# Kernel tuning notes

Hardware: AMD Instinct MI355X
Metric: run time of the kernel (lower is better)

## Reference

```python
import jax, jax.numpy as jnp
import numpy as np

NEG_SLOPE = 0.2
CONV3_NUM, CONV1_NUM, POLY_NUM = 3, 5, 4
FEAT_DIM = CONV3_NUM * 84 + CONV1_NUM * 12 + POLY_NUM * 12  # 360
DN = ('NCHW', 'OIHW', 'NCHW')


def leaky_relu(x):
    return jnp.where(x >= 0, x, NEG_SLOPE * x)


def conv3x3(x, feat):
    # per-sample dynamic 3x3 conv: feat[:, :81] -> kernel [3,3,3,3], feat[:, 81:84] -> bias
    B = x.shape[0]
    k = feat[:, :81].reshape(B, 3, 3, 3, 3)
    b = feat[:, 81:84]

    def one(xi, ki, bi):
        y = jax.lax.conv_general_dilated(xi[None], ki, (1, 1), 'SAME', dimension_numbers=DN)[0]
        return y + bi[:, None, None]

    return leaky_relu(jax.vmap(one)(x, k, b))


def conv1x1(x, feat):
    B = x.shape[0]
    k = feat[:, :9].reshape(B, 3, 3, 1, 1)
    b = feat[:, 9:12]

    def one(xi, ki, bi):
        y = jax.lax.conv_general_dilated(xi[None], ki, (1, 1), 'VALID', dimension_numbers=DN)[0]
        return y + bi[:, None, None]

    return leaky_relu(jax.vmap(one)(x, k, b))


def conv_stack(x, feature):
    residual = x
    for i in range(CONV3_NUM):
        x = conv3x3(x, feature[:, i * 84:(i + 1) * 84])
    off = CONV3_NUM * 84
    for i in range(CONV1_NUM):
        x = conv1x1(x, feature[:, off + i * 12:off + (i + 1) * 12])
    return residual + x


def att_map(feat, h_mat, w_mat, xc):
    # product over POLY_NUM of (a*h + b*w + c*x + d)
    att = jnp.ones_like(xc)
    for i in range(POLY_NUM):
        a = feat[:, i * 4 + 0].reshape(-1, 1, 1, 1)
        b = feat[:, i * 4 + 1].reshape(-1, 1, 1, 1)
        c = feat[:, i * 4 + 2].reshape(-1, 1, 1, 1)
        d = feat[:, i * 4 + 3].reshape(-1, 1, 1, 1)
        att = att * (a * h_mat + b * w_mat + c * xc + d)
    return att


def apply_attention(x, feature):
    H, W = x.shape[2], x.shape[3]
    h_mat = (jnp.arange(H, dtype=x.dtype) / H).reshape(1, 1, H, 1)
    w_mat = (jnp.arange(W, dtype=x.dtype) / W).reshape(1, 1, 1, W)
    off = CONV3_NUM * 84 + CONV1_NUM * 12
    atts = [att_map(feature[:, off + c * POLY_NUM * 4: off + (c + 1) * POLY_NUM * 4],
                    h_mat, w_mat, x[:, c:c + 1]) for c in range(3)]  # R, G, B
    att = jnp.concatenate(atts, axis=1)
    return x * (1 + att)


def setup_inputs() -> dict:
    key = jax.random.key(0)
    k1, k2, k3 = jax.random.split(key, 3)
    x = jax.random.uniform(k1, (8, 3, 512, 512), dtype=jnp.float32)
    thumb_x = jax.random.uniform(k2, (8, 3, 64, 64), dtype=jnp.float32)
    Wm = jax.random.normal(k3, (3, FEAT_DIM), dtype=jnp.float32) * 0.05
    bm = jnp.zeros((FEAT_DIM,), dtype=jnp.float32)
    return {"x": x, "thumb_x": thumb_x, "Wm": Wm, "bm": bm}


def reference(x, thumb_x, Wm, bm):
    # meta: GAP over thumbnail -> linear -> per-sample hypernetwork features [B, 360]
    feature = jnp.mean(thumb_x, axis=(2, 3)) @ Wm + bm
    x = conv_stack(x, feature)
    x = apply_attention(x, feature)
    thumb = conv_stack(thumb_x, feature)
    thumb = apply_attention(thumb, feature)
    return (x, thumb)
```

## Files before the change

kernel.cpp:

```cpp
#include <hip/hip_runtime.h>


typedef float v2f __attribute__((ext_vector_type(2)));
#define FMA2(a, b, c) __builtin_elementwise_fma((a), (b), (c))

__device__ __forceinline__ v2f leaky2(v2f v) {
    return __builtin_elementwise_max(v, v * 0.2f);
}

__device__ __forceinline__ v2f ldpair(const float* p) {
    v2f r; __builtin_memcpy(&r, p, 8); return r;
}
__device__ __forceinline__ void stpair(float* p, v2f v) {
    __builtin_memcpy(p, &v, 8);
}

constexpr int ROWS0 = 22;
constexpr int NCOLS = 73;
constexpr int CSTR  = 23;
constexpr int CHS   = NCOLS * CSTR;
constexpr int BUFSZ = 3 * CHS + 4;

__global__ __launch_bounds__(384) void prep_kernel(
    const float* __restrict__ thumb, const float* __restrict__ Wm,
    const float* __restrict__ bm, float* __restrict__ feat)
{
    const int b = blockIdx.x;
    const int t = threadIdx.x;
    const int ch = t >> 7;
    const int l  = t & 127;
    const float4* p = (const float4*)(thumb + (size_t)b * 3 * 4096);
    float s = 0.f;
#pragma unroll
    for (int k = 0; k < 8; ++k) {
        float4 v = p[ch * 1024 + l + k * 128];
        s += v.x + v.y + v.z + v.w;
    }
    __shared__ float red[384];
    red[t] = s;
    __syncthreads();
    for (int off = 64; off > 0; off >>= 1) {
        if (l < off) red[t] += red[t + off];
        __syncthreads();
    }
    if (t < 360) {
        const float sc = 1.f / 4096.f;
        const float m0 = red[0] * sc, m1 = red[128] * sc, m2 = red[256] * sc;
        feat[b * 360 + t] =
            fmaf(m0, Wm[t], fmaf(m1, Wm[360 + t], fmaf(m2, Wm[720 + t], bm[t])));
    }
}

__device__ __forceinline__ void conv_rows_pk(
    const float* __restrict__ buf, const float* __restrict__ fw,
    int r0, int gx, v2f acc[3][4])
{
    const float b0 = fw[81], b1 = fw[82], b2 = fw[83];
#pragma unroll
    for (int c = 0; c < 4; ++c) {
        v2f i0 = {b0, b0}; v2f i1 = {b1, b1}; v2f i2 = {b2, b2};
        acc[0][c] = i0; acc[1][c] = i1; acc[2][c] = i2;
    }
    const int c0 = (gx < 0) ? 3 : gx + 3;
    const int rb = r0 + 2;
#pragma unroll
    for (int ich = 0; ich < 3; ++ich) {
        const int base = ich * CHS + rb;
#pragma unroll
        for (int dy = 0; dy < 3; ++dy) {
            v2f win[6];
            win[0] = ldpair(&buf[base + c0 * CSTR + dy]);
#pragma unroll
            for (int k = 1; k < 6; ++k)
                win[k] = ldpair(&buf[base + (gx + 3 + k) * CSTR + dy]);
#pragma unroll
            for (int oc = 0; oc < 3; ++oc) {
                const float w0 = fw[oc * 27 + ich * 9 + dy * 3 + 0];
                const float w1 = fw[oc * 27 + ich * 9 + dy * 3 + 1];
                const float w2 = fw[oc * 27 + ich * 9 + dy * 3 + 2];
                v2f W0 = {w0, w0}; v2f W1 = {w1, w1}; v2f W2 = {w2, w2};
#pragma unroll
                for (int c = 0; c < 4; ++c) {
                    acc[oc][c] = FMA2(win[c], W0,
                                 FMA2(win[c + 1], W1,
                                 FMA2(win[c + 2], W2, acc[oc][c])));
                }
            }
        }
    }
}

__device__ __forceinline__ void write_strip_pk(
    float* __restrict__ buf, int r0, int gx, v2f acc[3][4])
{
#pragma unroll
    for (int oc = 0; oc < 3; ++oc)
#pragma unroll
        for (int c = 0; c < 4; ++c)
            stpair(&buf[oc * CHS + (gx + 4 + c) * CSTR + (r0 + 3)],
                   leaky2(acc[oc][c]));
}

__global__ __launch_bounds__(256, 4) void conv_att_kernel(
    const float* __restrict__ x, const float* __restrict__ thumb,
    const float* __restrict__ feat, float* __restrict__ out)
{
    __shared__ float buf[BUFSZ];

    int id = blockIdx.x;
    const float* src; float* dst; int H, W, b, trow, tcol;
    if (id < 2048) {
        b = id >> 8; const int t = id & 255;
        H = 512; W = 512; trow = (t >> 3) * 16; tcol = (t & 7) * 64;
        src = x; dst = out;
    } else {
        const int i2 = id - 2048;
        b = i2 >> 2; trow = (i2 & 3) * 16; tcol = 0;
        H = 64; W = 64; src = thumb;
        dst = out + (size_t)8 * 3 * 512 * 512;
    }
    const float* fb = feat + b * 360;
    const int tid = threadIdx.x;

    const float* sbg = src + (size_t)b * 3 * H * W;
    for (int q = tid; q < 1056; q += 256) {
        const int c = q / 352;
        const int rem = q - c * 352;
        const int mr = rem >> 4;
        const int k  = rem & 15;
        const int gr = trow + mr - 3;
        const int gc0 = tcol + 4 * k;
        float4 v = make_float4(0.f, 0.f, 0.f, 0.f);
        if ((unsigned)gr < (unsigned)H)
            v = *(const float4*)&sbg[(size_t)c * H * W + (size_t)gr * W + gc0];
        float* bp = &buf[c * CHS + (4 * k + 4) * CSTR + mr];
        bp[0] = v.x; bp[CSTR] = v.y; bp[2 * CSTR] = v.z; bp[3 * CSTR] = v.w;
    }
    if (tid < 132) {
        const int c = tid / 44;
        const int rem = tid - c * 44;
        const int mr = rem >> 1;
        const int side = rem & 1;
        const int gr = trow + mr - 3;
        const int gc0 = tcol + (side ? 64 : -4);
        const bool rok = (unsigned)gr < (unsigned)H;
        const float* gp = sbg + (size_t)c * H * W + (size_t)(rok ? gr : 0) * W;
        float4 v;
        if (rok && (unsigned)gc0 <= (unsigned)(W - 4)) {
            v = *(const float4*)&gp[gc0];
        } else {
            v.x = (rok && (unsigned)(gc0 + 0) < (unsigned)W) ? gp[gc0 + 0] : 0.f;
            v.y = (rok && (unsigned)(gc0 + 1) < (unsigned)W) ? gp[gc0 + 1] : 0.f;
            v.z = (rok && (unsigned)(gc0 + 2) < (unsigned)W) ? gp[gc0 + 2] : 0.f;
            v.w = (rok && (unsigned)(gc0 + 3) < (unsigned)W) ? gp[gc0 + 3] : 0.f;
        }
        float* bp = &buf[c * CHS + (side ? 68 : 0) * CSTR + mr];
        bp[0] = v.x; bp[CSTR] = v.y; bp[2 * CSTR] = v.z; bp[3 * CSTR] = v.w;
    }
    if (tid < 66) {
        const int c = tid / 22, mr = tid - c * 22;
        buf[c * CHS + 72 * CSTR + mr] = 0.f;
    }
    __syncthreads();

    const bool act1 = tid < 180;
    int s1, gx1;
    if (tid < 160) { s1 = tid >> 4; gx1 = 4 * (tid & 15); }
    else { const int v = tid - 160; s1 = v >> 1; gx1 = (v & 1) ? 64 : -4; }
    v2f acc[3][4];
    if (act1) conv_rows_pk(buf, fb, 2 * s1 - 2, gx1, acc);

    const int s3 = tid >> 4;
    const int gx3 = 4 * (tid & 15);
    v2f res2[3][4];
    if (tid < 128) {
#pragma unroll
        for (int ch = 0; ch < 3; ++ch)
#pragma unroll
            for (int c = 0; c < 4; ++c)
                res2[ch][c] = ldpair(&buf[ch * CHS + (gx3 + 4 + c) * CSTR + (2 * s3 + 3)]);
    }
    __syncthreads();

    if (act1) write_strip_pk(buf, 2 * s1 - 2, gx1, acc);
    __syncthreads();

    const bool act2 = tid < 162;
    int s2, gx2;
    if (tid < 144) { s2 = tid >> 4; gx2 = 4 * (tid & 15); }
    else { const int v = tid - 144; s2 = v >> 1; gx2 = (v & 1) ? 64 : -4; }
    if (act2) conv_rows_pk(buf, fb + 84, 2 * s2 - 1, gx2, acc);
    __syncthreads();

    if (act2) write_strip_pk(buf, 2 * s2 - 1, gx2, acc);
    __syncthreads();

    if (tid < 128) {
        v2f y[3][4];
        {
            v2f acc3[3][4];
            conv_rows_pk(buf, fb + 168, 2 * s3, gx3, acc3);
#pragma unroll
            for (int oc = 0; oc < 3; ++oc)
#pragma unroll
                for (int c = 0; c < 4; ++c) y[oc][c] = leaky2(acc3[oc][c]);
        }

#pragma unroll
        for (int lay = 0; lay < 5; ++lay) {
            const float* fw = fb + 252 + lay * 12;
            v2f W0 = {fw[0], fw[0]}; v2f W1 = {fw[1], fw[1]}; v2f W2 = {fw[2], fw[2]};
            v2f W3 = {fw[3], fw[3]}; v2f W4 = {fw[4], fw[4]}; v2f W5 = {fw[5], fw[5]};
            v2f W6 = {fw[6], fw[6]}; v2f W7 = {fw[7], fw[7]}; v2f W8 = {fw[8], fw[8]};
            v2f C0 = {fw[9], fw[9]}; v2f C1 = {fw[10], fw[10]}; v2f C2 = {fw[11], fw[11]};
            v2f z0[4], z1[4], z2[4];
#pragma unroll
            for (int c = 0; c < 4; ++c) {
                z0[c] = FMA2(y[0][c], W0, FMA2(y[1][c], W1, FMA2(y[2][c], W2, C0)));
                z1[c] = FMA2(y[0][c], W3, FMA2(y[1][c], W4, FMA2(y[2][c], W5, C1)));
                z2[c] = FMA2(y[0][c], W6, FMA2(y[1][c], W7, FMA2(y[2][c], W8, C2)));
            }
#pragma unroll
            for (int c = 0; c < 4; ++c) {
                y[0][c] = leaky2(z0[c]);
                y[1][c] = leaky2(z1[c]);
                y[2][c] = leaky2(z2[c]);
            }
        }

        const float invH = 1.f / (float)H;
        const float invW = 1.f / (float)W;
        const int gr0 = trow + 2 * s3;
        v2f h2 = {(float)gr0 * invH, (float)(gr0 + 1) * invH};
        const float wb = (float)(tcol + gx3) * invW;
        const v2f one = {1.f, 1.f};
#pragma unroll
        for (int ch = 0; ch < 3; ++ch) {
            const float* fp = fb + 312 + ch * 16;
            v2f PA0 = {fp[0], fp[0]},  PB0 = {fp[1], fp[1]},  PC0 = {fp[2], fp[2]},  PD0 = {fp[3], fp[3]};
            v2f PA1 = {fp[4], fp[4]},  PB1 = {fp[5], fp[5]},  PC1 = {fp[6], fp[6]},  PD1 = {fp[7], fp[7]};
            v2f PA2 = {fp[8], fp[8]},  PB2 = {fp[9], fp[9]},  PC2 = {fp[10], fp[10]}, PD2 = {fp[11], fp[11]};
            v2f PA3 = {fp[12], fp[12]}, PB3 = {fp[13], fp[13]}, PC3 = {fp[14], fp[14]}, PD3 = {fp[15], fp[15]};
            v2f t0 = FMA2(PA0, h2, PD0);
            v2f t1 = FMA2(PA1, h2, PD1);
            v2f t2 = FMA2(PA2, h2, PD2);
            v2f t3 = FMA2(PA3, h2, PD3);
            v2f o[4];
#pragma unroll
            for (int c = 0; c < 4; ++c) {
                const float wcs = wb + (float)c * invW;
                v2f Wc = {wcs, wcs};
                v2f v = y[ch][c] + res2[ch][c];
                v2f a = FMA2(PB0, Wc, FMA2(PC0, v, t0));
                a = a * FMA2(PB1, Wc, FMA2(PC1, v, t1));
                a = a * FMA2(PB2, Wc, FMA2(PC2, v, t2));
                a = a * FMA2(PB3, Wc, FMA2(PC3, v, t3));
                o[c] = v * (one + a);
            }
            float4 ra = make_float4(o[0].x, o[1].x, o[2].x, o[3].x);
            float4 rb = make_float4(o[0].y, o[1].y, o[2].y, o[3].y);
            float* dp = &dst[((size_t)(b * 3 + ch) * H + gr0) * W + tcol + gx3];
            *(float4*)dp = ra;
            *(float4*)(dp + W) = rb;
        }
    }
}

extern "C" void kernel_launch(void* const* d_in, const int* in_sizes, int n_in,
                              void* d_out, int out_size, void* d_ws, size_t ws_size,
                              hipStream_t stream) {
    const float* x = (const float*)d_in[0];
    const float* thumb = (const float*)d_in[1];
    const float* Wm = (const float*)d_in[2];
    const float* bm = (const float*)d_in[3];
    float* out = (float*)d_out;
    float* feat = (float*)d_ws;

    prep_kernel<<<8, 384, 0, stream>>>(thumb, Wm, bm, feat);
    conv_att_kernel<<<2080, 256, 0, stream>>>(x, thumb, feat, out);
}
```

Measured before the change: 111.7 us.

## Ping-pong conv layers between two shared buffers and batch global loads

Replaces the single in-place shared buffer with two buffers (A and B), so each 3x3 conv layer reads one and writes the other. This removes the extra barrier that was needed between computing and writing back each layer. The tile loads are also restructured so that all global float4 loads are issued into registers before any LDS stores, which improves memory-level parallelism. The cost is more shared memory per block, which could lower occupancy, plus more live registers during the load phase.

```diff
diff --git a/kernel.cpp b/kernel.cpp
--- a/kernel.cpp
+++ b/kernel.cpp
@@ -15,11 +15,13 @@
     __builtin_memcpy(p, &v, 8);
 }
 
-constexpr int ROWS0 = 22;
 constexpr int NCOLS = 73;
-constexpr int CSTR  = 23;
-constexpr int CHS   = NCOLS * CSTR;
-constexpr int BUFSZ = 3 * CHS + 4;
+constexpr int CSTRA = 23;
+constexpr int CHSA  = NCOLS * CSTRA;
+constexpr int ASZ   = 3 * CHSA + 4;
+constexpr int CSTRB = 21;
+constexpr int CHSB  = NCOLS * CSTRB;
+constexpr int BSZ   = 3 * CHSB + 4;
 
 __global__ __launch_bounds__(384) void prep_kernel(
     const float* __restrict__ thumb, const float* __restrict__ Wm,
@@ -51,9 +53,10 @@
     }
 }
 
+template<int CHS_, int CSTR_>
 __device__ __forceinline__ void conv_rows_pk(
     const float* __restrict__ buf, const float* __restrict__ fw,
-    int r0, int gx, v2f acc[3][4])
+    int rb, int gx, v2f acc[3][4])
 {
     const float b0 = fw[81], b1 = fw[82], b2 = fw[83];
 #pragma unroll
@@ -62,17 +65,16 @@
         acc[0][c] = i0; acc[1][c] = i1; acc[2][c] = i2;
     }
     const int c0 = (gx < 0) ? 3 : gx + 3;
-    const int rb = r0 + 2;
 #pragma unroll
     for (int ich = 0; ich < 3; ++ich) {
-        const int base = ich * CHS + rb;
+        const int base = ich * CHS_ + rb;
 #pragma unroll
         for (int dy = 0; dy < 3; ++dy) {
             v2f win[6];
-            win[0] = ldpair(&buf[base + c0 * CSTR + dy]);
+            win[0] = ldpair(&buf[base + c0 * CSTR_ + dy]);
 #pragma unroll
             for (int k = 1; k < 6; ++k)
-                win[k] = ldpair(&buf[base + (gx + 3 + k) * CSTR + dy]);
+                win[k] = ldpair(&buf[base + (gx + 3 + k) * CSTR_ + dy]);
 #pragma unroll
             for (int oc = 0; oc < 3; ++oc) {
                 const float w0 = fw[oc * 27 + ich * 9 + dy * 3 + 0];
@@ -90,22 +92,12 @@
     }
 }
 
-__device__ __forceinline__ void write_strip_pk(
-    float* __restrict__ buf, int r0, int gx, v2f acc[3][4])
-{
-#pragma unroll
-    for (int oc = 0; oc < 3; ++oc)
-#pragma unroll
-        for (int c = 0; c < 4; ++c)
-            stpair(&buf[oc * CHS + (gx + 4 + c) * CSTR + (r0 + 3)],
-                   leaky2(acc[oc][c]));
-}
-
 __global__ __launch_bounds__(256, 4) void conv_att_kernel(
     const float* __restrict__ x, const float* __restrict__ thumb,
     const float* __restrict__ feat, float* __restrict__ out)
 {
-    __shared__ float buf[BUFSZ];
+    __shared__ float bufA[ASZ];
+    __shared__ float bufB[BSZ];
 
     int id = blockIdx.x;
     const float* src; float* dst; int H, W, b, trow, tcol;
@@ -123,7 +115,10 @@
     const int tid = threadIdx.x;
 
     const float* sbg = src + (size_t)b * 3 * H * W;
-    for (int q = tid; q < 1056; q += 256) {
+    float4 stv[4];
+#pragma unroll
+    for (int i = 0; i < 4; ++i) {
+        const int q = tid + 256 * i;
         const int c = q / 352;
         const int rem = q - c * 352;
         const int mr = rem >> 4;
@@ -133,42 +128,72 @@
         float4 v = make_float4(0.f, 0.f, 0.f, 0.f);
         if ((unsigned)gr < (unsigned)H)
             v = *(const float4*)&sbg[(size_t)c * H * W + (size_t)gr * W + gc0];
-        float* bp = &buf[c * CHS + (4 * k + 4) * CSTR + mr];
-        bp[0] = v.x; bp[CSTR] = v.y; bp[2 * CSTR] = v.z; bp[3 * CSTR] = v.w;
-    }
-    if (tid < 132) {
-        const int c = tid / 44;
-        const int rem = tid - c * 44;
-        const int mr = rem >> 1;
-        const int side = rem & 1;
+        stv[i] = v;
+    }
+    const bool has5 = tid < 32;
+    float4 st5 = make_float4(0.f, 0.f, 0.f, 0.f);
+    if (has5) {
+        const int q = tid + 1024;
+        const int rem = q - 704;
+        const int mr = rem >> 4;
+        const int k  = rem & 15;
         const int gr = trow + mr - 3;
-        const int gc0 = tcol + (side ? 64 : -4);
+        const int gc0 = tcol + 4 * k;
+        if ((unsigned)gr < (unsigned)H)
+            st5 = *(const float4*)&sbg[(size_t)2 * H * W + (size_t)gr * W + gc0];
+    }
+    const bool hasH = tid < 132;
+    float4 hv = make_float4(0.f, 0.f, 0.f, 0.f);
+    int hc = 0, hmr = 0, hside = 0;
+    if (hasH) {
+        hc = tid / 44;
+        const int rem = tid - hc * 44;
+        hmr = rem >> 1;
+        hside = rem & 1;
+        const int gr = trow + hmr - 3;
+        const int gc0 = tcol + (hside ? 64 : -4);
         const bool rok = (unsigned)gr < (unsigned)H;
-        const float* gp = sbg + (size_t)c * H * W + (size_t)(rok ? gr : 0) * W;
-        float4 v;
+        const float* gp = sbg + (size_t)hc * H * W + (size_t)(rok ? gr : 0) * W;
         if (rok && (unsigned)gc0 <= (unsigned)(W - 4)) {
-            v = *(const float4*)&gp[gc0];
+            hv = *(const float4*)&gp[gc0];
         } else {
-            v.x = (rok && (unsigned)(gc0 + 0) < (unsigned)W) ? gp[gc0 + 0] : 0.f;
-            v.y = (rok && (unsigned)(gc0 + 1) < (unsigned)W) ? gp[gc0 + 1] : 0.f;
-            v.z = (rok && (unsigned)(gc0 + 2) < (unsigned)W) ? gp[gc0 + 2] : 0.f;
-            v.w = (rok && (unsigned)(gc0 + 3) < (unsigned)W) ? gp[gc0 + 3] : 0.f;
-        }
-        float* bp = &buf[c * CHS + (side ? 68 : 0) * CSTR + mr];
-        bp[0] = v.x; bp[CSTR] = v.y; bp[2 * CSTR] = v.z; bp[3 * CSTR] = v.w;
+            hv.x = (rok && (unsigned)(gc0 + 0) < (unsigned)W) ? gp[gc0 + 0] : 0.f;
+            hv.y = (rok && (unsigned)(gc0 + 1) < (unsigned)W) ? gp[gc0 + 1] : 0.f;
+            hv.z = (rok && (unsigned)(gc0 + 2) < (unsigned)W) ? gp[gc0 + 2] : 0.f;
+            hv.w = (rok && (unsigned)(gc0 + 3) < (unsigned)W) ? gp[gc0 + 3] : 0.f;
+        }
+    }
+#pragma unroll
+    for (int i = 0; i < 4; ++i) {
+        const int q = tid + 256 * i;
+        const int c = q / 352;
+        const int rem = q - c * 352;
+        const int mr = rem >> 4;
+        const int k  = rem & 15;
+        float* bp = &bufA[c * CHSA + (4 * k + 4) * CSTRA + mr];
+        bp[0] = stv[i].x; bp[CSTRA] = stv[i].y;
+        bp[2 * CSTRA] = stv[i].z; bp[3 * CSTRA] = stv[i].w;
+    }
+    if (has5) {
+        const int rem = tid + 1024 - 704;
+        const int mr = rem >> 4;
+        const int k  = rem & 15;
+        float* bp = &bufA[2 * CHSA + (4 * k + 4) * CSTRA + mr];
+        bp[0] = st5.x; bp[CSTRA] = st5.y; bp[2 * CSTRA] = st5.z; bp[3 * CSTRA] = st5.w;
+    }
+    if (hasH) {
+        float* bp = &bufA[hc * CHSA + (hside ? 68 : 0) * CSTRA + hmr];
+        bp[0] = hv.x; bp[CSTRA] = hv.y; bp[2 * CSTRA] = hv.z; bp[3 * CSTRA] = hv.w;
     }
     if (tid < 66) {
         const int c = tid / 22, mr = tid - c * 22;
-        buf[c * CHS + 72 * CSTR + mr] = 0.f;
+        bufA[c * CHSA + 72 * CSTRA + mr] = 0.f;
+    } else if (tid < 126) {
+        const int t2 = tid - 66;
+        const int c = t2 / 20, r = t2 - c * 20;
+        bufB[c * CHSB + 72 * CSTRB + r] = 0.f;
     }
     __syncthreads();
-
-    const bool act1 = tid < 180;
-    int s1, gx1;
-    if (tid < 160) { s1 = tid >> 4; gx1 = 4 * (tid & 15); }
-    else { const int v = tid - 160; s1 = v >> 1; gx1 = (v & 1) ? 64 : -4; }
-    v2f acc[3][4];
-    if (act1) conv_rows_pk(buf, fb, 2 * s1 - 2, gx1, acc);
 
     const int s3 = tid >> 4;
     const int gx3 = 4 * (tid & 15);
@@ -178,28 +203,49 @@
         for (int ch = 0; ch < 3; ++ch)
 #pragma unroll
             for (int c = 0; c < 4; ++c)
-                res2[ch][c] = ldpair(&buf[ch * CHS + (gx3 + 4 + c) * CSTR + (2 * s3 + 3)]);
+                res2[ch][c] = ldpair(&bufA[ch * CHSA + (gx3 + 4 + c) * CSTRA + (2 * s3 + 3)]);
+    }
+    {
+        const bool act1 = tid < 180;
+        int s1, gx1;
+        if (tid < 160) { s1 = tid >> 4; gx1 = 4 * (tid & 15); }
+        else { const int v = tid - 160; s1 = v >> 1; gx1 = (v & 1) ? 64 : -4; }
+        if (act1) {
+            v2f acc[3][4];
+            conv_rows_pk<CHSA, CSTRA>(bufA, fb, 2 * s1, gx1, acc);
+#pragma unroll
+            for (int oc = 0; oc < 3; ++oc)
+#pragma unroll
+                for (int c = 0; c < 4; ++c)
+                    stpair(&bufB[oc * CHSB + (gx1 + 4 + c) * CSTRB + 2 * s1],
+                           leaky2(acc[oc][c]));
+        }
     }
     __syncthreads();
 
-    if (act1) write_strip_pk(buf, 2 * s1 - 2, gx1, acc);
-    __syncthreads();
-
-    const bool act2 = tid < 162;
-    int s2, gx2;
-    if (tid < 144) { s2 = tid >> 4; gx2 = 4 * (tid & 15); }
-    else { const int v = tid - 144; s2 = v >> 1; gx2 = (v & 1) ? 64 : -4; }
-    if (act2) conv_rows_pk(buf, fb + 84, 2 * s2 - 1, gx2, acc);
-    __syncthreads();
-
-    if (act2) write_strip_pk(buf, 2 * s2 - 1, gx2, acc);
+    {
+        const bool act2 = tid < 162;
+        int s2, gx2;
+        if (tid < 144) { s2 = tid >> 4; gx2 = 4 * (tid & 15); }
+        else { const int v = tid - 144; s2 = v >> 1; gx2 = (v & 1) ? 64 : -4; }
+        if (act2) {
+            v2f acc[3][4];
+            conv_rows_pk<CHSB, CSTRB>(bufB, fb + 84, 2 * s2, gx2, acc);
+#pragma unroll
+            for (int oc = 0; oc < 3; ++oc)
+#pragma unroll
+                for (int c = 0; c < 4; ++c)
+                    stpair(&bufA[oc * CHSA + (gx2 + 4 + c) * CSTRA + 2 * s2 + 2],
+                           leaky2(acc[oc][c]));
+        }
+    }
     __syncthreads();
 
     if (tid < 128) {
         v2f y[3][4];
         {
             v2f acc3[3][4];
-            conv_rows_pk(buf, fb + 168, 2 * s3, gx3, acc3);
+            conv_rows_pk<CHSA, CSTRA>(bufA, fb + 168, 2 * s3 + 2, gx3, acc3);
 #pragma unroll
             for (int oc = 0; oc < 3; ++oc)
 #pragma unroll
```

New measurement: 110.3 us. No clear change (-1.3%).
